# Performance work log

Measured on AMD Instinct MI355X. Metric: run time of the kernel, lower is better.

## Reference

```python
import jax, jax.numpy as jnp
import numpy as np

BETA = 0.5
OT_ITER = 50
OT_K = 1
EPS = 1e-5


def _l2norm(x, eps=EPS):
    n = jnp.linalg.norm(x, axis=-1, keepdims=True)
    return x / jnp.maximum(n, eps)


def cost_matrix_cosine(x, y):
    # [B,M,D],[B,N,D] -> [B,M,N] cosine distance
    return 1.0 - jnp.einsum('bmd,bnd->bmn', _l2norm(x), _l2norm(y))


def ipot(C, x_len, x_pad, y_pad, y_len, joint_pad, beta, iteration, k):
    # C: [B,M,N] (already detached). Returns transport plan T: [B,N,M].
    b, m, n = C.shape
    jp_t = jnp.swapaxes(joint_pad, 1, 2)                      # [B,N,M]
    sigma = jnp.where(x_pad, 0.0, 1.0 / x_len[:, None])       # [B,M]
    sigma = sigma[:, :, None]                                 # [B,M,1]
    T = jnp.where(jp_t, 0.0, 1.0).astype(C.dtype)             # [B,N,M]
    A = jnp.where(jp_t, 0.0, jnp.exp(-jnp.swapaxes(C, 1, 2) / beta))
    x_mask = (x_pad.astype(C.dtype) * 1e4)[:, None, :]        # [B,1,M]
    y_mask = (y_pad.astype(C.dtype) * 1e4)[:, None, :]        # [B,1,N]
    xl = x_len[:, None, None]
    yl = y_len[:, None, None]

    def outer(carry, _):
        T, sigma = carry
        Q = A * T                                             # [B,N,M]

        def inner(sig, _):
            # sig: [B,M,1]
            delta = 1.0 / (yl * jnp.swapaxes(Q @ sig, 1, 2) + y_mask)   # [B,1,N]
            sig_new = 1.0 / (xl * (delta @ Q) + x_mask)                 # [B,1,M]
            return jnp.swapaxes(sig_new, 1, 2), delta

        sigma, deltas = jax.lax.scan(inner, sigma, None, length=k)
        delta = deltas[-1]                                    # [B,1,N]
        T_new = jnp.swapaxes(delta, 1, 2) * Q * jnp.swapaxes(sigma, 1, 2)
        return (T_new, sigma), None

    (T, _), _ = jax.lax.scan(outer, (T, sigma), None, length=iteration)
    return jnp.where(jp_t, 0.0, T)


def optimal_transport_dist(txt_emb, img_emb, txt_pad, img_pad,
                           beta=BETA, iteration=OT_ITER, k=OT_K):
    cost = cost_matrix_cosine(txt_emb, img_emb)               # [B,M,N]
    joint_pad = txt_pad[:, :, None] | img_pad[:, None, :]
    cost = jnp.where(joint_pad, 0.0, cost)
    txt_len = (txt_pad.shape[1] - txt_pad.sum(1)).astype(cost.dtype)
    img_len = (img_pad.shape[1] - img_pad.sum(1)).astype(cost.dtype)
    T = ipot(jax.lax.stop_gradient(cost), txt_len, txt_pad, img_pad,
             img_len, joint_pad, beta, iteration, k)
    T = jax.lax.stop_gradient(T)
    # trace(cost @ T)  == einsum over matching indices
    return jnp.einsum('bmn,bnm->b', cost, T)


def crf_llh(emissions, tags, mask, start_transitions, end_transitions, transitions):
    # emissions [T,B,K], tags [T,B] int, mask [T,B] bool (mask[0] all True)
    T, B, K = emissions.shape
    b_idx = jnp.arange(B)
    maskf = mask.astype(emissions.dtype)

    # numerator: gold path score
    score = start_transitions[tags[0]] + emissions[0, b_idx, tags[0]]
    trans_sc = transitions[tags[:-1], tags[1:]] * maskf[1:]              # [T-1,B]
    emit_sc = jnp.take_along_axis(emissions[1:], tags[1:][..., None], axis=-1)[..., 0] * maskf[1:]
    score = score + trans_sc.sum(0) + emit_sc.sum(0)
    seq_ends = mask.astype(jnp.int32).sum(0) - 1
    last_tags = tags[seq_ends, b_idx]
    numerator = score + end_transitions[last_tags]

    # denominator: forward algorithm (log-sum-exp recurrence)
    def step(s, inp):
        emis_t, mask_t = inp
        nxt = jax.nn.logsumexp(s[:, :, None] + transitions[None] + emis_t[:, None, :], axis=1)
        return jnp.where(mask_t[:, None], nxt, s), None

    init = start_transitions[None, :] + emissions[0]                     # [B,K]
    final, _ = jax.lax.scan(step, init, (emissions[1:], mask[1:]))
    denominator = jax.nn.logsumexp(final + end_transitions[None, :], axis=1)
    return numerator - denominator                                       # [B]


def setup_inputs() -> dict:
    key = jax.random.key(0)
    ks = jax.random.split(key, 10)
    T, B, K = 512, 64, 21
    M, N, D = 512, 512, 768

    emissions = jax.random.normal(ks[0], (T, B, K), dtype=jnp.float32)
    txt_emb = jax.random.normal(ks[1], (B, M, D), dtype=jnp.float32)
    img_emb = jax.random.normal(ks[2], (B, N, D), dtype=jnp.float32)

    start_transitions = jax.random.uniform(ks[3], (K,), minval=-0.1, maxval=0.1)
    end_transitions = jax.random.uniform(ks[4], (K,), minval=-0.1, maxval=0.1)
    transitions = jax.random.uniform(ks[5], (K, K), minval=-0.1, maxval=0.1)

    tags = jax.random.randint(ks[6], (T, B), 0, K)
    crf_len = jax.random.randint(ks[7], (B,), T // 2, T + 1)
    crf_mask = jnp.arange(T)[:, None] < crf_len[None, :]   # mask[0] all True
    txt_len = jax.random.randint(ks[8], (B,), M // 2, M + 1)
    txt_pad = jnp.arange(M)[None, :] >= txt_len[:, None]
    img_len = jax.random.randint(ks[9], (B,), N // 2, N + 1)
    img_pad = jnp.arange(N)[None, :] >= img_len[:, None]

    return {
        'emissions': emissions, 'txt_emb': txt_emb, 'img_emb': img_emb,
        'start_transitions': start_transitions, 'end_transitions': end_transitions,
        'transitions': transitions, 'tags': tags, 'crf_mask': crf_mask,
        'txt_pad': txt_pad, 'img_pad': img_pad,
    }


def reference(emissions, txt_emb, img_emb, start_transitions, end_transitions,
              transitions, tags, crf_mask, txt_pad, img_pad):
    llh = crf_llh(emissions, tags, crf_mask, start_transitions,
                  end_transitions, transitions)              # [B]
    ot = optimal_transport_dist(txt_emb, img_emb, txt_pad, img_pad)  # [B]
    loss = -llh.sum() + ot.sum()
    return loss
```

## Files before the change

kernel.cpp:

```cpp
#include <hip/hip_runtime.h>
#include <stdint.h>

typedef unsigned short u16;
typedef unsigned char u8;
typedef unsigned int u32;

#define LOG2E 1.4426950408889634f
#define LN2   0.6931471805599453f

typedef __attribute__((ext_vector_type(2))) float f32x2;

__device__ __forceinline__ float exp2_(float x){ return __builtin_amdgcn_exp2f(x); }
__device__ __forceinline__ float log2_(float x){ return __builtin_amdgcn_logf(x); }
__device__ __forceinline__ float bflo(u32 u){ return __uint_as_float(u << 16); }
__device__ __forceinline__ float bfhi(u32 u){ return __uint_as_float(u & 0xffff0000u); }
__device__ __forceinline__ u16 f2bf(float f){
  u32 u = __float_as_uint(f);
  return (u16)((u + 0x7fffu + ((u >> 16) & 1u)) >> 16);
}
__device__ __forceinline__ u32 pkbf(float lo, float hi){
  u32 r; asm("v_cvt_pk_bf16_f32 %0, %1, %2" : "=v"(r) : "v"(lo), "v"(hi)); return r;
}
__device__ __forceinline__ int rdmask(const u8* p, int i, int st){ return (int)p[(size_t)i * st]; }

__global__ void k_detect(const u32* __restrict__ cmask, int* __restrict__ flags) {
  flags[0] = (cmask[0] == 0x01010101u) ? 1 : 4;
}

__global__ __launch_bounds__(256) void k_normalize(const float* __restrict__ txt,
                                                   const float* __restrict__ img,
                                                   u16* __restrict__ xh, u16* __restrict__ yh) {
  int row = blockIdx.x * 4 + (threadIdx.x >> 6);
  int l = threadIdx.x & 63;
  const float* src; u16* dst;
  if (row < 32768) { src = txt + (size_t)row * 768; dst = xh + (size_t)row * 768; }
  else { int r2 = row - 32768; src = img + (size_t)r2 * 768; dst = yh + (size_t)r2 * 768; }
  float v[12]; float ss = 0.f;
  #pragma unroll
  for (int s = 0; s < 12; ++s) { v[s] = src[l + (s << 6)]; ss = fmaf(v[s], v[s], ss); }
  #pragma unroll
  for (int off = 32; off; off >>= 1) ss += __shfl_xor(ss, off);
  float sc = 1.0f / fmaxf(sqrtf(ss), 1e-5f);
  #pragma unroll
  for (int s = 0; s < 12; ++s) dst[l + (s << 6)] = f2bf(v[s] * sc);
}

typedef __attribute__((ext_vector_type(8))) short short8;
typedef __attribute__((ext_vector_type(4))) float f32x4;

__global__ __launch_bounds__(256) void k_gemm_crf(const u16* __restrict__ xh, const u16* __restrict__ yh,
                                                  const u8* __restrict__ xpad, const u8* __restrict__ ypad,
                                                  const int* __restrict__ flags,
                                                  u16* __restrict__ Ct2,
                                                  const float* __restrict__ emis, const int* __restrict__ tags,
                                                  const u8* __restrict__ mask,
                                                  const float* __restrict__ startT, const float* __restrict__ endT,
                                                  const float* __restrict__ trans, float* __restrict__ llh) {
  __shared__ u16 As[128 * 64];
  __shared__ u16 Bs[128 * 64];
  __shared__ float tr[441];
  int st = flags[0];
  int bt = blockIdx.x;
  int tid = threadIdx.x;

  if (bt >= 1024) {
    int b = bt - 1024;
    for (int i = tid; i < 441; i += 256) tr[i] = trans[i];
    __syncthreads();
    if (tid >= 64) return;
    int k = tid;
    float accs = 0.f; int cnt = 0;
    for (int t = k; t < 512; t += 64) {
      int mt = rdmask(mask, (t << 6) + b, st);
      cnt += mt;
      int tg = tags[(t << 6) + b];
      if (t == 0) {
        accs += startT[tg] + emis[(size_t)b * 21 + tg];
      } else if (mt) {
        int tgp = tags[((t - 1) << 6) + b];
        accs += tr[tgp * 21 + tg] + emis[((size_t)((t << 6) + b)) * 21 + tg];
      }
    }
    #pragma unroll
    for (int off = 32; off; off >>= 1) { accs += __shfl_down(accs, off); cnt += __shfl_down(cnt, off); }
    float numer = 0.f;
    if (k == 0) {
      int last = tags[((cnt - 1) << 6) + b];
      numer = accs + endT[last];
    }
    int kc = (k < 21) ? k : 20;
    float s = startT[kc] + emis[(size_t)b * 21 + kc];
    for (int t = 1; t < 512; ++t) {
      float z[21];
      float zmax = -3.0e38f;
      #pragma unroll
      for (int j = 0; j < 21; ++j) {
        float sj = __shfl(s, j);
        z[j] = sj + tr[j * 21 + kc];
        zmax = fmaxf(zmax, z[j]);
      }
      float sum = 0.f;
      #pragma unroll
      for (int j = 0; j < 21; ++j) sum += exp2_((z[j] - zmax) * LOG2E);
      float ns = zmax + log2_(sum) * LN2 + emis[((size_t)((t << 6) + b)) * 21 + kc];
      s = rdmask(mask, (t << 6) + b, st) ? ns : s;
    }
    float f = (k < 21) ? (s + endT[kc]) : -3.0e38f;
    float m = f;
    #pragma unroll
    for (int off = 32; off; off >>= 1) m = fmaxf(m, __shfl_xor(m, off));
    float sum = (k < 21) ? exp2_((f - m) * LOG2E) : 0.f;
    #pragma unroll
    for (int off = 32; off; off >>= 1) sum += __shfl_xor(sum, off);
    float denom = m + log2_(sum) * LN2;
    if (k == 0) llh[b] = numer - denom;
    return;
  }

  int b = bt >> 4;
  int tile = bt & 15;
  int tn = tile >> 2, tm = tile & 3;
  const u16* Ab = yh + ((size_t)b * 512 + tn * 128) * 768;
  const u16* Bb = xh + ((size_t)b * 512 + tm * 128) * 768;
  int w = tid >> 6, l = tid & 63;
  int wr = (w >> 1) << 6, wc = (w & 1) << 6;
  f32x4 acc[4][4] = {};
  for (int k0 = 0; k0 < 768; k0 += 64) {
    #pragma unroll
    for (int q = 0; q < 4; ++q) {
      int slot = (q << 8) + tid;
      int row = slot >> 3, col = (slot & 7) << 3;
      uint4 va = *(const uint4*)(Ab + row * 768 + k0 + col);
      uint4 vb = *(const uint4*)(Bb + row * 768 + k0 + col);
      *(uint4*)((char*)As + slot * 16) = va;
      *(uint4*)((char*)Bs + slot * 16) = vb;
    }
    __syncthreads();
    #pragma unroll
    for (int kk = 0; kk < 64; kk += 32) {
      int cb = (kk + ((l >> 4) << 3)) * 2;
      short8 a[4], bb[4];
      #pragma unroll
      for (int i = 0; i < 4; ++i)
        a[i] = *(const short8*)((const char*)As + (wr + (i << 4) + (l & 15)) * 128 + cb);
      #pragma unroll
      for (int j = 0; j < 4; ++j)
        bb[j] = *(const short8*)((const char*)Bs + (wc + (j << 4) + (l & 15)) * 128 + cb);
      #pragma unroll
      for (int i = 0; i < 4; ++i)
        #pragma unroll
        for (int j = 0; j < 4; ++j)
          acc[i][j] = __builtin_amdgcn_mfma_f32_16x16x32_bf16(a[i], bb[j], acc[i][j], 0, 0, 0);
    }
    __syncthreads();
  }
  int n0 = (tn << 7) + wr, m0 = (tm << 7) + wc;
  #pragma unroll
  for (int i = 0; i < 4; ++i) {
    #pragma unroll
    for (int j = 0; j < 4; ++j) {
      int m = m0 + (j << 4) + (l & 15);
      int xpm = rdmask(xpad, b * 512 + m, st);
      #pragma unroll
      for (int r = 0; r < 4; ++r) {
        int n = n0 + (i << 4) + ((l >> 4) << 2) + r;
        float v = 2.8853901f * (1.0f - acc[i][j][r]);
        if (xpm | rdmask(ypad, b * 512 + n, st)) v = 30000.0f;
        Ct2[((size_t)(b * 512 + n) << 9) + m] = f2bf(v);
      }
    }
  }
}

__device__ __forceinline__ void batch_barrier(int* cnt, int target) {
  __syncthreads();
  if (threadIdx.x == 0) {
    __hip_atomic_fetch_add(cnt, 1, __ATOMIC_RELEASE, __HIP_MEMORY_SCOPE_AGENT);
    while (__hip_atomic_load(cnt, __ATOMIC_ACQUIRE, __HIP_MEMORY_SCOPE_AGENT) < target)
      __builtin_amdgcn_s_sleep(1);
  }
  __syncthreads();
}

__global__ __launch_bounds__(1024)
void k_ipot_f8(const u16* __restrict__ Ct2,
               const u8* __restrict__ xpad, const u8* __restrict__ ypad,
               const int* __restrict__ flags,
               int* __restrict__ gcount, float* __restrict__ c_part,
               float* __restrict__ fin_part,
               float* __restrict__ ot) {
  __shared__ __align__(16) u32  A_l[128 * 128];
  __shared__ __align__(16) float cpart[4][512];
  __shared__ __align__(16) float sig[512];
  __shared__ __align__(16) float xmk[512];
  __shared__ __align__(16) float ymk[512];
  __shared__ float redw[16];
  __shared__ int cnti[2];

  int bid = blockIdx.x;
  int b = bid & 63, p = bid >> 6;
  int tid = threadIdx.x;
  int w = tid >> 6, l = tid & 63;
  int st = flags[0];

  if (tid < 2) cnti[tid] = 0;
  __syncthreads();
  if (tid < 512) {
    int xp = rdmask(xpad, (b << 9) + tid, st) ? 1 : 0;
    int yp = rdmask(ypad, (b << 9) + tid, st) ? 1 : 0;
    xmk[tid] = xp ? 1e4f : 0.f;
    ymk[tid] = yp ? 1e4f : 0.f;
    atomicAdd(&cnti[0], 1 - xp);
    atomicAdd(&cnti[1], 1 - yp);
  }
  __syncthreads();
  float xl = (float)cnti[0], yl = (float)cnti[1];
  if (tid < 512) sig[tid] = (xmk[tid] > 0.f) ? 0.f : (1.0f / xl);

  const int base_n = p << 7;
  const int row0 = (w << 3);
  const u16* Cb = Ct2 + ((size_t)(b * 512 + base_n) << 9);
  int* cnt_b = gcount + (b << 6);
  float* cp_b = c_part + ((size_t)b << 12);

  u32 Tp[32];
  #pragma unroll
  for (int r = 0; r < 8; ++r) {
    const uint4 cv = *(const uint4*)(Cb + (size_t)(row0 + r) * 512 + (l << 3));
    float a0 = exp2_(-bflo(cv.x)), a1 = exp2_(-bfhi(cv.x));
    float a2 = exp2_(-bflo(cv.y)), a3 = exp2_(-bfhi(cv.y));
    float a4 = exp2_(-bflo(cv.z)), a5 = exp2_(-bfhi(cv.z));
    float a6 = exp2_(-bflo(cv.w)), a7 = exp2_(-bfhi(cv.w));
    u32 w0 = (u32)__builtin_amdgcn_cvt_pk_fp8_f32(a0, a1, 0, false);
    w0 = (u32)__builtin_amdgcn_cvt_pk_fp8_f32(a2, a3, (int)w0, true);
    u32 w1 = (u32)__builtin_amdgcn_cvt_pk_fp8_f32(a4, a5, 0, false);
    w1 = (u32)__builtin_amdgcn_cvt_pk_fp8_f32(a6, a7, (int)w1, true);
    uint2 wv; wv.x = w0; wv.y = w1;
    *(uint2*)(A_l + (row0 + r) * 128 + (l << 1)) = wv;
    Tp[r * 4 + 0] = 0x3F803F80u;
    Tp[r * 4 + 1] = 0x3F803F80u;
    Tp[r * 4 + 2] = 0x3F803F80u;
    Tp[r * 4 + 3] = 0x3F803F80u;
  }
  __syncthreads();

  for (int it = 1; it <= 50; ++it) {
    int par = it & 1;
    float dl[8];
    {
      float sg[8];
      const float4* ps = (const float4*)&sig[l << 3];
      float4 s0 = ps[0], s1 = ps[1];
      sg[0]=s0.x; sg[1]=s0.y; sg[2]=s0.z; sg[3]=s0.w;
      sg[4]=s1.x; sg[5]=s1.y; sg[6]=s1.z; sg[7]=s1.w;
      #pragma unroll
      for (int r = 0; r < 8; ++r) {
        const uint2 av = *(const uint2*)(A_l + (row0 + r) * 128 + (l << 1));
        f32x2 a01 = __builtin_amdgcn_cvt_pk_f32_fp8((int)av.x, false);
        f32x2 a23 = __builtin_amdgcn_cvt_pk_f32_fp8((int)av.x, true);
        f32x2 a45 = __builtin_amdgcn_cvt_pk_f32_fp8((int)av.y, false);
        f32x2 a67 = __builtin_amdgcn_cvt_pk_f32_fp8((int)av.y, true);
        float acc = 0.f;
        { u32 tw = Tp[r*4+0]; float q0 = a01.x*bflo(tw), q1 = a01.y*bfhi(tw);
          Tp[r*4+0] = pkbf(q0,q1); acc = fmaf(q0,sg[0],acc); acc = fmaf(q1,sg[1],acc); }
        { u32 tw = Tp[r*4+1]; float q0 = a23.x*bflo(tw), q1 = a23.y*bfhi(tw);
          Tp[r*4+1] = pkbf(q0,q1); acc = fmaf(q0,sg[2],acc); acc = fmaf(q1,sg[3],acc); }
        { u32 tw = Tp[r*4+2]; float q0 = a45.x*bflo(tw), q1 = a45.y*bfhi(tw);
          Tp[r*4+2] = pkbf(q0,q1); acc = fmaf(q0,sg[4],acc); acc = fmaf(q1,sg[5],acc); }
        { u32 tw = Tp[r*4+3]; float q0 = a67.x*bflo(tw), q1 = a67.y*bfhi(tw);
          Tp[r*4+3] = pkbf(q0,q1); acc = fmaf(q0,sg[6],acc); acc = fmaf(q1,sg[7],acc); }
        #pragma unroll
        for (int off = 32; off; off >>= 1) acc += __shfl_xor(acc, off);
        dl[r] = 1.0f / fmaf(yl, acc, ymk[base_n + row0 + r]);
      }
    }
    {
      float cp[8] = {0.f,0.f,0.f,0.f,0.f,0.f,0.f,0.f};
      #pragma unroll
      for (int r = 0; r < 8; ++r) {
        float d = dl[r];
        { u32 tw = Tp[r*4+0]; cp[0] = fmaf(bflo(tw),d,cp[0]); cp[1] = fmaf(bfhi(tw),d,cp[1]); }
        { u32 tw = Tp[r*4+1]; cp[2] = fmaf(bflo(tw),d,cp[2]); cp[3] = fmaf(bfhi(tw),d,cp[3]); }
        { u32 tw = Tp[r*4+2]; cp[4] = fmaf(bflo(tw),d,cp[4]); cp[5] = fmaf(bfhi(tw),d,cp[5]); }
        { u32 tw = Tp[r*4+3]; cp[6] = fmaf(bflo(tw),d,cp[6]); cp[7] = fmaf(bfhi(tw),d,cp[7]); }
      }
      float4 v0, v1;
      v0.x=cp[0]; v0.y=cp[1]; v0.z=cp[2]; v0.w=cp[3];
      v1.x=cp[4]; v1.y=cp[5]; v1.z=cp[6]; v1.w=cp[7];
      float4* dst = (float4*)&cpart[w & 3][l << 3];
      if (w < 4) { dst[0] = v0; dst[1] = v1; }
      __syncthreads();
      if (w >= 4 && w < 8) {
        float4 o0 = dst[0], o1 = dst[1];
        o0.x+=v0.x; o0.y+=v0.y; o0.z+=v0.z; o0.w+=v0.w;
        o1.x+=v1.x; o1.y+=v1.y; o1.z+=v1.z; o1.w+=v1.w;
        dst[0] = o0; dst[1] = o1;
      }
      __syncthreads();
      if (w >= 8 && w < 12) {
        float4 o0 = dst[0], o1 = dst[1];
        o0.x+=v0.x; o0.y+=v0.y; o0.z+=v0.z; o0.w+=v0.w;
        o1.x+=v1.x; o1.y+=v1.y; o1.z+=v1.z; o1.w+=v1.w;
        dst[0] = o0; dst[1] = o1;
      }
      __syncthreads();
      if (w >= 12) {
        float4 o0 = dst[0], o1 = dst[1];
        o0.x+=v0.x; o0.y+=v0.y; o0.z+=v0.z; o0.w+=v0.w;
        o1.x+=v1.x; o1.y+=v1.y; o1.z+=v1.z; o1.w+=v1.w;
        dst[0] = o0; dst[1] = o1;
      }
      __syncthreads();
    }
    if (tid < 512) {
      float s = cpart[0][tid] + cpart[1][tid] + cpart[2][tid] + cpart[3][tid];
      __hip_atomic_store(&cp_b[(par << 11) + (p << 9) + tid], s, __ATOMIC_RELAXED, __HIP_MEMORY_SCOPE_AGENT);
    }
    batch_barrier(&cnt_b[it - 1], 4);
    if (tid < 512) {
      const float* basep = cp_b + (par << 11);
      float s = __hip_atomic_load(&basep[tid], __ATOMIC_RELAXED, __HIP_MEMORY_SCOPE_AGENT);
      s += __hip_atomic_load(&basep[512 + tid], __ATOMIC_RELAXED, __HIP_MEMORY_SCOPE_AGENT);
      s += __hip_atomic_load(&basep[1024 + tid], __ATOMIC_RELAXED, __HIP_MEMORY_SCOPE_AGENT);
      s += __hip_atomic_load(&basep[1536 + tid], __ATOMIC_RELAXED, __HIP_MEMORY_SCOPE_AGENT);
      sig[tid] = 1.0f / fmaf(xl, s, xmk[tid]);
    }
    __syncthreads();
    {
      float sg[8];
      const float4* ps = (const float4*)&sig[l << 3];
      float4 s0 = ps[0], s1 = ps[1];
      sg[0]=s0.x; sg[1]=s0.y; sg[2]=s0.z; sg[3]=s0.w;
      sg[4]=s1.x; sg[5]=s1.y; sg[6]=s1.z; sg[7]=s1.w;
      #pragma unroll
      for (int r = 0; r < 8; ++r) {
        float d = dl[r];
        { u32 tw = Tp[r*4+0]; Tp[r*4+0] = pkbf(bflo(tw)*d*sg[0], bfhi(tw)*d*sg[1]); }
        { u32 tw = Tp[r*4+1]; Tp[r*4+1] = pkbf(bflo(tw)*d*sg[2], bfhi(tw)*d*sg[3]); }
        { u32 tw = Tp[r*4+2]; Tp[r*4+2] = pkbf(bflo(tw)*d*sg[4], bfhi(tw)*d*sg[5]); }
        { u32 tw = Tp[r*4+3]; Tp[r*4+3] = pkbf(bflo(tw)*d*sg[6], bfhi(tw)*d*sg[7]); }
      }
    }
  }

  float accT = 0.f;
  #pragma unroll
  for (int r = 0; r < 8; ++r) {
    const uint4 cv = *(const uint4*)(Cb + (size_t)(row0 + r) * 512 + (l << 3));
    { u32 tw = Tp[r*4+0]; accT = fmaf(bflo(cv.x), bflo(tw), accT); accT = fmaf(bfhi(cv.x), bfhi(tw), accT); }
    { u32 tw = Tp[r*4+1]; accT = fmaf(bflo(cv.y), bflo(tw), accT); accT = fmaf(bfhi(cv.y), bfhi(tw), accT); }
    { u32 tw = Tp[r*4+2]; accT = fmaf(bflo(cv.z), bflo(tw), accT); accT = fmaf(bfhi(cv.z), bfhi(tw), accT); }
    { u32 tw = Tp[r*4+3]; accT = fmaf(bflo(cv.w), bflo(tw), accT); accT = fmaf(bfhi(cv.w), bfhi(tw), accT); }
  }
  #pragma unroll
  for (int off = 32; off; off >>= 1) accT += __shfl_xor(accT, off);
  if (l == 0) redw[w] = accT;
  __syncthreads();
  if (tid == 0) {
    float s = 0.f;
    #pragma unroll
    for (int ww = 0; ww < 16; ++ww) s += redw[ww];
    __hip_atomic_store(&fin_part[(b << 2) + p], s, __ATOMIC_RELAXED, __HIP_MEMORY_SCOPE_AGENT);
  }
  batch_barrier(&cnt_b[50], 4);
  if (p == 0 && tid == 0) {
    float s = 0.f;
    #pragma unroll
    for (int pp = 0; pp < 4; ++pp)
      s += __hip_atomic_load(&fin_part[(b << 2) + pp], __ATOMIC_RELAXED, __HIP_MEMORY_SCOPE_AGENT);
    ot[b] = s * 0.34657359f;
  }
}

__global__ __launch_bounds__(64) void k_finalize(const float* __restrict__ llh, const float* __restrict__ ot,
                                                 float* __restrict__ out) {
  int l = threadIdx.x;
  float v = ot[l] - llh[l];
  #pragma unroll
  for (int off = 32; off; off >>= 1) v += __shfl_down(v, off);
  if (l == 0) out[0] = v;
}

extern "C" void kernel_launch(void* const* d_in, const int* in_sizes, int n_in,
                              void* d_out, int out_size, void* d_ws, size_t ws_size,
                              hipStream_t stream) {
  const float* emis  = (const float*)d_in[0];
  const float* txt   = (const float*)d_in[1];
  const float* img   = (const float*)d_in[2];
  const float* startT= (const float*)d_in[3];
  const float* endT  = (const float*)d_in[4];
  const float* trans = (const float*)d_in[5];
  const int*  tags   = (const int*)d_in[6];
  const u8* cmask = (const u8*)d_in[7];
  const u8* xpad  = (const u8*)d_in[8];
  const u8* ypad  = (const u8*)d_in[9];
  char* wsb = (char*)d_ws;
  u16* xh  = (u16*)wsb;
  u16* yh  = (u16*)(wsb + 50331648ll);
  u16* Ct2 = (u16*)(wsb + 100663296ll);
  float* ot    = (float*)(wsb + 134217728ll);
  float* llh   = ot + 64;
  int*  flags  = (int*)(llh + 64);
  int*  gcount = (int*)(wsb + 134218752ll);
  float* c_part= (float*)(wsb + 134235136ll);
  float* fin_part=(float*)(wsb + 135283712ll);
  float* out = (float*)d_out;

  hipMemsetAsync(gcount, 0, 64 * 64 * sizeof(int), stream);
  hipLaunchKernelGGL(k_detect, dim3(1), dim3(1), 0, stream, (const u32*)cmask, flags);
  hipLaunchKernelGGL(k_normalize, dim3(16384), dim3(256), 0, stream, txt, img, xh, yh);
  hipLaunchKernelGGL(k_gemm_crf, dim3(1088), dim3(256), 0, stream, xh, yh, xpad, ypad, flags, Ct2,
                     emis, tags, cmask, startT, endT, trans, llh);
  hipLaunchKernelGGL(k_ipot_f8, dim3(256), dim3(1024), 0, stream,
                     Ct2, xpad, ypad, flags, gcount, c_part, fin_part, ot);
  hipLaunchKernelGGL(k_finalize, dim3(1), dim3(64), 0, stream, llh, ot, out);
}
```

Measured before the change: 803.4 us.

## Split each batch's IPOT work across eight blocks instead of four

Each batch is now handled by eight 1024-thread blocks of 64 rows each rather than four blocks of 128 rows, so 512 blocks cover the GPU's CUs instead of 256. This halves per-thread register state and shortens each iteration's critical path. The row-sum pass is fused into the column pass using the freshly computed Q values, and the intra-block reduction drops from four barriers to two. In exchange, every iteration's cross-block barrier must wait for eight blocks, and each block loads eight partial vectors. The gcount, c_part and fin_part scratch buffers are moved to the start of the workspace, overlapping xh, which is why their memset now runs after the GEMM kernel.

New measurement: 1.272 ms. 58.3% more time.

```diff
diff --git a/kernel.cpp b/kernel.cpp
--- a/kernel.cpp
+++ b/kernel.cpp
@@ -183,14 +183,14 @@
 }
 
 __global__ __launch_bounds__(1024)
-void k_ipot_f8(const u16* __restrict__ Ct2,
+void k_ipot8f8(const u16* __restrict__ Ct2,
                const u8* __restrict__ xpad, const u8* __restrict__ ypad,
                const int* __restrict__ flags,
                int* __restrict__ gcount, float* __restrict__ c_part,
                float* __restrict__ fin_part,
                float* __restrict__ ot) {
-  __shared__ __align__(16) u32  A_l[128 * 128];
-  __shared__ __align__(16) float cpart[4][512];
+  __shared__ __align__(16) u32  A_l[64 * 128];
+  __shared__ __align__(16) float cpart[8][512];
   __shared__ __align__(16) float sig[512];
   __shared__ __align__(16) float xmk[512];
   __shared__ __align__(16) float ymk[512];
@@ -198,7 +198,7 @@
   __shared__ int cnti[2];
 
   int bid = blockIdx.x;
-  int b = bid & 63, p = bid >> 6;
+  int b = bid >> 3, p = bid & 7;
   int tid = threadIdx.x;
   int w = tid >> 6, l = tid & 63;
   int st = flags[0];
@@ -217,15 +217,15 @@
   float xl = (float)cnti[0], yl = (float)cnti[1];
   if (tid < 512) sig[tid] = (xmk[tid] > 0.f) ? 0.f : (1.0f / xl);
 
-  const int base_n = p << 7;
-  const int row0 = (w << 3);
+  const int base_n = p << 6;
+  const int row0 = (w << 2);
   const u16* Cb = Ct2 + ((size_t)(b * 512 + base_n) << 9);
   int* cnt_b = gcount + (b << 6);
-  float* cp_b = c_part + ((size_t)b << 12);
-
-  u32 Tp[32];
-  #pragma unroll
-  for (int r = 0; r < 8; ++r) {
+  float* cp_b = c_part + (size_t)b * 8192;
+
+  u32 Tp[16];
+  #pragma unroll
+  for (int r = 0; r < 4; ++r) {
     const uint4 cv = *(const uint4*)(Cb + (size_t)(row0 + r) * 512 + (l << 3));
     float a0 = exp2_(-bflo(cv.x)), a1 = exp2_(-bfhi(cv.x));
     float a2 = exp2_(-bflo(cv.y)), a3 = exp2_(-bfhi(cv.y));
@@ -246,7 +246,8 @@
 
   for (int it = 1; it <= 50; ++it) {
     int par = it & 1;
-    float dl[8];
+    float dl[4];
+    float cp[8] = {0.f,0.f,0.f,0.f,0.f,0.f,0.f,0.f};
     {
       float sg[8];
       const float4* ps = (const float4*)&sig[l << 3];
@@ -254,75 +255,58 @@
       sg[0]=s0.x; sg[1]=s0.y; sg[2]=s0.z; sg[3]=s0.w;
       sg[4]=s1.x; sg[5]=s1.y; sg[6]=s1.z; sg[7]=s1.w;
       #pragma unroll
-      for (int r = 0; r < 8; ++r) {
+      for (int r = 0; r < 4; ++r) {
         const uint2 av = *(const uint2*)(A_l + (row0 + r) * 128 + (l << 1));
         f32x2 a01 = __builtin_amdgcn_cvt_pk_f32_fp8((int)av.x, false);
         f32x2 a23 = __builtin_amdgcn_cvt_pk_f32_fp8((int)av.x, true);
         f32x2 a45 = __builtin_amdgcn_cvt_pk_f32_fp8((int)av.y, false);
         f32x2 a67 = __builtin_amdgcn_cvt_pk_f32_fp8((int)av.y, true);
+        float q[8];
         float acc = 0.f;
-        { u32 tw = Tp[r*4+0]; float q0 = a01.x*bflo(tw), q1 = a01.y*bfhi(tw);
-          Tp[r*4+0] = pkbf(q0,q1); acc = fmaf(q0,sg[0],acc); acc = fmaf(q1,sg[1],acc); }
-        { u32 tw = Tp[r*4+1]; float q0 = a23.x*bflo(tw), q1 = a23.y*bfhi(tw);
-          Tp[r*4+1] = pkbf(q0,q1); acc = fmaf(q0,sg[2],acc); acc = fmaf(q1,sg[3],acc); }
-        { u32 tw = Tp[r*4+2]; float q0 = a45.x*bflo(tw), q1 = a45.y*bfhi(tw);
-          Tp[r*4+2] = pkbf(q0,q1); acc = fmaf(q0,sg[4],acc); acc = fmaf(q1,sg[5],acc); }
-        { u32 tw = Tp[r*4+3]; float q0 = a67.x*bflo(tw), q1 = a67.y*bfhi(tw);
-          Tp[r*4+3] = pkbf(q0,q1); acc = fmaf(q0,sg[6],acc); acc = fmaf(q1,sg[7],acc); }
+        { u32 tw = Tp[r*4+0]; q[0] = a01.x*bflo(tw); q[1] = a01.y*bfhi(tw);
+          Tp[r*4+0] = pkbf(q[0],q[1]); acc = fmaf(q[0],sg[0],acc); acc = fmaf(q[1],sg[1],acc); }
+        { u32 tw = Tp[r*4+1]; q[2] = a23.x*bflo(tw); q[3] = a23.y*bfhi(tw);
+          Tp[r*4+1] = pkbf(q[2],q[3]); acc = fmaf(q[2],sg[2],acc); acc = fmaf(q[3],sg[3],acc); }
+        { u32 tw = Tp[r*4+2]; q[4] = a45.x*bflo(tw); q[5] = a45.y*bfhi(tw);
+          Tp[r*4+2] = pkbf(q[4],q[5]); acc = fmaf(q[4],sg[4],acc); acc = fmaf(q[5],sg[5],acc); }
+        { u32 tw = Tp[r*4+3]; q[6] = a67.x*bflo(tw); q[7] = a67.y*bfhi(tw);
+          Tp[r*4+3] = pkbf(q[6],q[7]); acc = fmaf(q[6],sg[6],acc); acc = fmaf(q[7],sg[7],acc); }
         #pragma unroll
         for (int off = 32; off; off >>= 1) acc += __shfl_xor(acc, off);
-        dl[r] = 1.0f / fmaf(yl, acc, ymk[base_n + row0 + r]);
+        float d = 1.0f / fmaf(yl, acc, ymk[base_n + row0 + r]);
+        dl[r] = d;
+        #pragma unroll
+        for (int c = 0; c < 8; ++c) cp[c] = fmaf(d, q[c], cp[c]);
       }
     }
     {
-      float cp[8] = {0.f,0.f,0.f,0.f,0.f,0.f,0.f,0.f};
-      #pragma unroll
-      for (int r = 0; r < 8; ++r) {
-        float d = dl[r];
-        { u32 tw = Tp[r*4+0]; cp[0] = fmaf(bflo(tw),d,cp[0]); cp[1] = fmaf(bfhi(tw),d,cp[1]); }
-        { u32 tw = Tp[r*4+1]; cp[2] = fmaf(bflo(tw),d,cp[2]); cp[3] = fmaf(bfhi(tw),d,cp[3]); }
-        { u32 tw = Tp[r*4+2]; cp[4] = fmaf(bflo(tw),d,cp[4]); cp[5] = fmaf(bfhi(tw),d,cp[5]); }
-        { u32 tw = Tp[r*4+3]; cp[6] = fmaf(bflo(tw),d,cp[6]); cp[7] = fmaf(bfhi(tw),d,cp[7]); }
-      }
       float4 v0, v1;
       v0.x=cp[0]; v0.y=cp[1]; v0.z=cp[2]; v0.w=cp[3];
       v1.x=cp[4]; v1.y=cp[5]; v1.z=cp[6]; v1.w=cp[7];
-      float4* dst = (float4*)&cpart[w & 3][l << 3];
-      if (w < 4) { dst[0] = v0; dst[1] = v1; }
+      float4* dst = (float4*)&cpart[w & 7][l << 3];
+      if (w < 8) { dst[0] = v0; dst[1] = v1; }
       __syncthreads();
-      if (w >= 4 && w < 8) {
+      if (w >= 8) {
         float4 o0 = dst[0], o1 = dst[1];
         o0.x+=v0.x; o0.y+=v0.y; o0.z+=v0.z; o0.w+=v0.w;
         o1.x+=v1.x; o1.y+=v1.y; o1.z+=v1.z; o1.w+=v1.w;
         dst[0] = o0; dst[1] = o1;
       }
       __syncthreads();
-      if (w >= 8 && w < 12) {
-        float4 o0 = dst[0], o1 = dst[1];
-        o0.x+=v0.x; o0.y+=v0.y; o0.z+=v0.z; o0.w+=v0.w;
-        o1.x+=v1.x; o1.y+=v1.y; o1.z+=v1.z; o1.w+=v1.w;
-        dst[0] = o0; dst[1] = o1;
-      }
-      __syncthreads();
-      if (w >= 12) {
-        float4 o0 = dst[0], o1 = dst[1];
-        o0.x+=v0.x; o0.y+=v0.y; o0.z+=v0.z; o0.w+=v0.w;
-        o1.x+=v1.x; o1.y+=v1.y; o1.z+=v1.z; o1.w+=v1.w;
-        dst[0] = o0; dst[1] = o1;
-      }
-      __syncthreads();
     }
     if (tid < 512) {
-      float s = cpart[0][tid] + cpart[1][tid] + cpart[2][tid] + cpart[3][tid];
-      __hip_atomic_store(&cp_b[(par << 11) + (p << 9) + tid], s, __ATOMIC_RELAXED, __HIP_MEMORY_SCOPE_AGENT);
-    }
-    batch_barrier(&cnt_b[it - 1], 4);
+      float s = 0.f;
+      #pragma unroll
+      for (int k = 0; k < 8; ++k) s += cpart[k][tid];
+      __hip_atomic_store(&cp_b[(par << 12) + (p << 9) + tid], s, __ATOMIC_RELAXED, __HIP_MEMORY_SCOPE_AGENT);
+    }
+    batch_barrier(&cnt_b[it - 1], 8);
     if (tid < 512) {
-      const float* basep = cp_b + (par << 11);
-      float s = __hip_atomic_load(&basep[tid], __ATOMIC_RELAXED, __HIP_MEMORY_SCOPE_AGENT);
-      s += __hip_atomic_load(&basep[512 + tid], __ATOMIC_RELAXED, __HIP_MEMORY_SCOPE_AGENT);
-      s += __hip_atomic_load(&basep[1024 + tid], __ATOMIC_RELAXED, __HIP_MEMORY_SCOPE_AGENT);
-      s += __hip_atomic_load(&basep[1536 + tid], __ATOMIC_RELAXED, __HIP_MEMORY_SCOPE_AGENT);
+      const float* basep = cp_b + (par << 12);
+      float s = 0.f;
+      #pragma unroll
+      for (int pp = 0; pp < 8; ++pp)
+        s += __hip_atomic_load(&basep[(pp << 9) + tid], __ATOMIC_RELAXED, __HIP_MEMORY_SCOPE_AGENT);
       sig[tid] = 1.0f / fmaf(xl, s, xmk[tid]);
     }
     __syncthreads();
@@ -333,7 +317,7 @@
       sg[0]=s0.x; sg[1]=s0.y; sg[2]=s0.z; sg[3]=s0.w;
       sg[4]=s1.x; sg[5]=s1.y; sg[6]=s1.z; sg[7]=s1.w;
       #pragma unroll
-      for (int r = 0; r < 8; ++r) {
+      for (int r = 0; r < 4; ++r) {
         float d = dl[r];
         { u32 tw = Tp[r*4+0]; Tp[r*4+0] = pkbf(bflo(tw)*d*sg[0], bfhi(tw)*d*sg[1]); }
         { u32 tw = Tp[r*4+1]; Tp[r*4+1] = pkbf(bflo(tw)*d*sg[2], bfhi(tw)*d*sg[3]); }
@@ -345,7 +329,7 @@
 
   float accT = 0.f;
   #pragma unroll
-  for (int r = 0; r < 8; ++r) {
+  for (int r = 0; r < 4; ++r) {
     const uint4 cv = *(const uint4*)(Cb + (size_t)(row0 + r) * 512 + (l << 3));
     { u32 tw = Tp[r*4+0]; accT = fmaf(bflo(cv.x), bflo(tw), accT); accT = fmaf(bfhi(cv.x), bfhi(tw), accT); }
     { u32 tw = Tp[r*4+1]; accT = fmaf(bflo(cv.y), bflo(tw), accT); accT = fmaf(bfhi(cv.y), bfhi(tw), accT); }
@@ -360,14 +344,14 @@
     float s = 0.f;
     #pragma unroll
     for (int ww = 0; ww < 16; ++ww) s += redw[ww];
-    __hip_atomic_store(&fin_part[(b << 2) + p], s, __ATOMIC_RELAXED, __HIP_MEMORY_SCOPE_AGENT);
-  }
-  batch_barrier(&cnt_b[50], 4);
+    __hip_atomic_store(&fin_part[(b << 3) + p], s, __ATOMIC_RELAXED, __HIP_MEMORY_SCOPE_AGENT);
+  }
+  batch_barrier(&cnt_b[50], 8);
   if (p == 0 && tid == 0) {
     float s = 0.f;
     #pragma unroll
-    for (int pp = 0; pp < 4; ++pp)
-      s += __hip_atomic_load(&fin_part[(b << 2) + pp], __ATOMIC_RELAXED, __HIP_MEMORY_SCOPE_AGENT);
+    for (int pp = 0; pp < 8; ++pp)
+      s += __hip_atomic_load(&fin_part[(b << 3) + pp], __ATOMIC_RELAXED, __HIP_MEMORY_SCOPE_AGENT);
     ot[b] = s * 0.34657359f;
   }
 }
@@ -401,17 +385,17 @@
   float* ot    = (float*)(wsb + 134217728ll);
   float* llh   = ot + 64;
   int*  flags  = (int*)(llh + 64);
-  int*  gcount = (int*)(wsb + 134218752ll);
-  float* c_part= (float*)(wsb + 134235136ll);
-  float* fin_part=(float*)(wsb + 135283712ll);
+  int*  gcount  = (int*)wsb;
+  float* c_part = (float*)(wsb + 16384ll);
+  float* fin_part=(float*)(wsb + 16384ll + 2097152ll);
   float* out = (float*)d_out;
 
-  hipMemsetAsync(gcount, 0, 64 * 64 * sizeof(int), stream);
   hipLaunchKernelGGL(k_detect, dim3(1), dim3(1), 0, stream, (const u32*)cmask, flags);
   hipLaunchKernelGGL(k_normalize, dim3(16384), dim3(256), 0, stream, txt, img, xh, yh);
   hipLaunchKernelGGL(k_gemm_crf, dim3(1088), dim3(256), 0, stream, xh, yh, xpad, ypad, flags, Ct2,
                      emis, tags, cmask, startT, endT, trans, llh);
-  hipLaunchKernelGGL(k_ipot_f8, dim3(256), dim3(1024), 0, stream,
+  hipMemsetAsync(gcount, 0, 64 * 64 * sizeof(int), stream);
+  hipLaunchKernelGGL(k_ipot8f8, dim3(512), dim3(1024), 0, stream,
                      Ct2, xpad, ypad, flags, gcount, c_part, fin_part, ot);
   hipLaunchKernelGGL(k_finalize, dim3(1), dim3(64), 0, stream, llh, ot, out);
 }
```
